# Performance work log

Measured on AMD Instinct MI355X. Metric: run time of the kernel, lower is better.

## Reference

```python
import jax, jax.numpy as jnp
import numpy as np

# dims: B batch, T query len, S kv len (=T, self-attn prefill), D embed,
# N query heads, K kv heads, G = N//K GQA groups, H head dim
B, T, D = 2, 2048, 2048
N, K, H = 16, 4, 128
G = N // K
MIN_TS, MAX_TS = 1.0, 10000.0
W_SCALE = 0.02


def _rope(x, pos):
    # x: [B, L, heads, H]; pos: [B, L] int
    half = x.shape[-1] // 2
    frac = (2.0 * jnp.arange(half, dtype=jnp.float32)) / (2 * half)
    timescale = MIN_TS * (MAX_TS / MIN_TS) ** frac            # [half]
    sinusoid = pos[:, :, None, None].astype(jnp.float32) / timescale  # [B,L,1,half]
    sin = jnp.sin(sinusoid).astype(x.dtype)
    cos = jnp.cos(sinusoid).astype(x.dtype)
    x1, x2 = jnp.split(x, 2, axis=-1)
    return jnp.concatenate([x1 * cos - x2 * sin, x2 * cos + x1 * sin], axis=-1)


def setup_inputs() -> dict:
    key = jax.random.key(0)
    ks = jax.random.split(key, 6)
    Xq = jax.random.normal(ks[0], (B, T, D), dtype=jnp.float32)
    Xkv = jax.random.normal(ks[1], (B, T, D), dtype=jnp.float32)
    pos = jnp.tile(jnp.arange(T, dtype=jnp.int32)[None, :], (B, 1))
    Wq = jax.random.normal(ks[2], (D, N, H), dtype=jnp.float32) * W_SCALE
    Wk = jax.random.normal(ks[3], (D, K, H), dtype=jnp.float32) * W_SCALE
    Wv = jax.random.normal(ks[4], (D, K, H), dtype=jnp.float32) * W_SCALE
    Wo = jax.random.normal(ks[5], (N, H, D), dtype=jnp.float32) * W_SCALE
    return {"Xq": Xq, "Xkv": Xkv, "q_positions": pos, "kv_positions": pos,
            "Wq": Wq, "Wk": Wk, "Wv": Wv, "Wo": Wo}


def reference(Xq, Xkv, q_positions, kv_positions, Wq, Wk, Wv, Wo):
    # QKV projections (tensordot in torch == einsum over contracted axis)
    q = _rope(jnp.einsum('btd,dnh->btnh', Xq, Wq), q_positions)   # [B,T,N,H]
    k = _rope(jnp.einsum('bsd,dkh->bskh', Xkv, Wk), kv_positions)  # [B,S,K,H]
    v = jnp.einsum('bsd,dkh->bskh', Xkv, Wv)                       # [B,S,K,H]
    # GQA: query head n = kv_head*G + group (matches torch enable_gqa repeat_interleave)
    qg = q.reshape(B, T, K, G, H)
    # SDPA with explicit scale=1.0 (as in the original), causal mask
    scores = jnp.einsum('btkgh,bskh->bkgts', qg, k)                # [B,K,G,T,S]
    causal = jnp.tril(jnp.ones((T, T), dtype=bool))
    scores = jnp.where(causal, scores, jnp.finfo(scores.dtype).min)
    probs = jax.nn.softmax(scores, axis=-1)
    attn = jnp.einsum('bkgts,bskh->btkgh', probs, v).reshape(B, T, N, H)
    # o_proj contracts both (N, H) axes
    return jnp.einsum('btnh,nhd->btd', attn, Wo)
```

## Files before the change

kernel.cpp:

```cpp
#include <hip/hip_runtime.h>
#include <stdint.h>

#define Bb 2
#define Td 2048
#define Sd 2048
#define Dd 2048
#define Nh 16
#define Kvh 4
#define Hd 128

typedef unsigned short u16;
typedef short bf16x8 __attribute__((ext_vector_type(8)));
typedef float f32x4 __attribute__((ext_vector_type(4)));

__device__ __forceinline__ u16 f2bf(float f) {
  union { float f; unsigned u; } v; v.f = f;
  v.u += 0x7FFF + ((v.u >> 16) & 1);
  return (u16)(v.u >> 16);
}
__device__ __forceinline__ float bf2f(u16 h) {
  union { unsigned u; float f; } v; v.u = ((unsigned)h) << 16;
  return v.f;
}

__global__ __launch_bounds__(256) void k_convert(const float* __restrict__ in,
                                                 u16* __restrict__ out, int n8) {
  int i = blockIdx.x * 256 + threadIdx.x;
  if (i >= n8) return;
  const float4* p = (const float4*)in;
  float4 a = p[(size_t)i * 2], b = p[(size_t)i * 2 + 1];
  ushort4 r0, r1;
  r0.x = f2bf(a.x); r0.y = f2bf(a.y); r0.z = f2bf(a.z); r0.w = f2bf(a.w);
  r1.x = f2bf(b.x); r1.y = f2bf(b.y); r1.z = f2bf(b.z); r1.w = f2bf(b.w);
  ((ushort4*)out)[(size_t)i * 2] = r0;
  ((ushort4*)out)[(size_t)i * 2 + 1] = r1;
}

__global__ __launch_bounds__(256) void k_transpose_f32_bf16(const float* __restrict__ in,
                                                            u16* __restrict__ out,
                                                            int R, int C) {
  __shared__ u16 tile[32][33];
  int c0 = blockIdx.x * 32, r0 = blockIdx.y * 32;
  int tx = threadIdx.x & 31, ty = threadIdx.x >> 5;
#pragma unroll
  for (int i = 0; i < 32; i += 8)
    tile[ty + i][tx] = f2bf(in[(size_t)(r0 + ty + i) * C + c0 + tx]);
  __syncthreads();
#pragma unroll
  for (int i = 0; i < 32; i += 8)
    out[(size_t)(c0 + ty + i) * R + r0 + tx] = tile[tx][ty + i];
}

__global__ __launch_bounds__(256) void k_transpose_v(const u16* __restrict__ in,
                                                     u16* __restrict__ out) {
  __shared__ u16 tile[32][33];
  int bkh = blockIdx.z;
  int b = bkh >> 2, kh = bkh & 3;
  int h0 = blockIdx.x * 32, s0 = blockIdx.y * 32;
  int tx = threadIdx.x & 31, ty = threadIdx.x >> 5;
  const u16* ib = in + (size_t)b * Sd * (Kvh * Hd) + kh * Hd;
  u16* ob = out + (size_t)(b * Kvh + kh) * Hd * Sd;
#pragma unroll
  for (int i = 0; i < 32; i += 8)
    tile[ty + i][tx] = ib[(size_t)(s0 + ty + i) * (Kvh * Hd) + h0 + tx];
  __syncthreads();
#pragma unroll
  for (int i = 0; i < 32; i += 8)
    ob[(size_t)(h0 + ty + i) * Sd + s0 + tx] = tile[tx][ty + i];
}

__global__ __launch_bounds__(256) void k_rope_tables(const int* __restrict__ pos,
                                                     float* __restrict__ cosT,
                                                     float* __restrict__ sinT, int total) {
  int idx = blockIdx.x * 256 + threadIdx.x;
  if (idx >= total) return;
  int i = idx & 63, bt = idx >> 6;
  float p = (float)pos[bt];
  float ts = powf(10000.0f, (float)i * (1.0f / 64.0f));
  float x = p / ts;
  cosT[idx] = cosf(x);
  sinT[idx] = sinf(x);
}

__global__ __launch_bounds__(256) void k_rope_q(float* __restrict__ x,
                                                const float* __restrict__ cosT,
                                                const float* __restrict__ sinT, int total) {
  int idx = blockIdx.x * 256 + threadIdx.x;
  if (idx >= total) return;
  int i = idx & 63;
  int nh = (idx >> 6) % Nh;
  int bt = idx / (64 * Nh);
  size_t base = ((size_t)bt * Nh + nh) * Hd;
  float c = cosT[bt * 64 + i], s = sinT[bt * 64 + i];
  float x1 = x[base + i], x2 = x[base + 64 + i];
  x[base + i]      = x1 * c - x2 * s;
  x[base + 64 + i] = x2 * c + x1 * s;
}

__global__ __launch_bounds__(256) void k_rope_k(const float* __restrict__ x,
                                                u16* __restrict__ out,
                                                const float* __restrict__ cosT,
                                                const float* __restrict__ sinT, int total) {
  int idx = blockIdx.x * 256 + threadIdx.x;
  if (idx >= total) return;
  int i = idx & 63;
  int kh = (idx >> 6) % Kvh;
  int bt = idx / (64 * Kvh);
  int b = bt >> 11, s = bt & 2047;
  size_t bi = ((size_t)bt * Kvh + kh) * Hd;
  size_t bo = (((size_t)b * Kvh + kh) * Sd + s) * Hd;
  float c = cosT[bt * 64 + i], sn = sinT[bt * 64 + i];
  float x1 = x[bi + i], x2 = x[bi + 64 + i];
  out[bo + i]      = f2bf(x1 * c - x2 * sn);
  out[bo + 64 + i] = f2bf(x2 * c + x1 * sn);
}

template <int OUT_F32>
__global__ __launch_bounds__(256) void k_gemm_bt(const u16* __restrict__ A,
                                                 const u16* __restrict__ Bt,
                                                 void* __restrict__ C,
                                                 int M, int Ncols, int Kd) {
  __shared__ u16 lA[128 * 32];
  __shared__ u16 lB[128 * 32];
  int tiles_n = Ncols >> 7;
  int bm = blockIdx.x / tiles_n, bn = blockIdx.x % tiles_n;
  int tid = threadIdx.x;
  int lane = tid & 63, wave = tid >> 6;
  int wr = wave >> 1, wc = wave & 1;
  int e0 = tid * 8;
  int r0 = e0 >> 5, c0 = e0 & 31;
  int lr = lane & 15, hi = lane >> 4;
  int kq = hi * 8;

  const u16* gA = A + (size_t)(bm * 128 + r0) * Kd + c0;
  const u16* gB = Bt + (size_t)(bn * 128 + r0) * Kd + c0;

  f32x4 acc[4][4] = {};

  for (int k0 = 0; k0 < Kd; k0 += 32) {
    __syncthreads();
    __builtin_amdgcn_global_load_lds(
        (const __attribute__((address_space(1))) uint32_t*)(gA + k0),
        (__attribute__((address_space(3))) uint32_t*)&lA[e0], 16, 0, 0);
    __builtin_amdgcn_global_load_lds(
        (const __attribute__((address_space(1))) uint32_t*)(gA + k0 + (size_t)64 * Kd),
        (__attribute__((address_space(3))) uint32_t*)&lA[e0 + 64 * 32], 16, 0, 0);
    __builtin_amdgcn_global_load_lds(
        (const __attribute__((address_space(1))) uint32_t*)(gB + k0),
        (__attribute__((address_space(3))) uint32_t*)&lB[e0], 16, 0, 0);
    __builtin_amdgcn_global_load_lds(
        (const __attribute__((address_space(1))) uint32_t*)(gB + k0 + (size_t)64 * Kd),
        (__attribute__((address_space(3))) uint32_t*)&lB[e0 + 64 * 32], 16, 0, 0);
    __syncthreads();

    bf16x8 af[4], bfr[4];
#pragma unroll
    for (int m = 0; m < 4; ++m)
      af[m] = *(const bf16x8*)&lA[(wr * 64 + m * 16 + lr) * 32 + kq];
#pragma unroll
    for (int n = 0; n < 4; ++n)
      bfr[n] = *(const bf16x8*)&lB[(wc * 64 + n * 16 + lr) * 32 + kq];
#pragma unroll
    for (int m = 0; m < 4; ++m)
#pragma unroll
      for (int n = 0; n < 4; ++n)
        acc[m][n] = __builtin_amdgcn_mfma_f32_16x16x32_bf16(af[m], bfr[n], acc[m][n], 0, 0, 0);
  }

  int orow0 = bm * 128 + wr * 64 + hi * 4;
  int ocol0 = bn * 128 + wc * 64 + lr;
#pragma unroll
  for (int m = 0; m < 4; ++m)
#pragma unroll
    for (int n = 0; n < 4; ++n)
#pragma unroll
      for (int q = 0; q < 4; ++q) {
        size_t idx = (size_t)(orow0 + m * 16 + q) * Ncols + ocol0 + n * 16;
        if (OUT_F32) ((float*)C)[idx] = acc[m][n][q];
        else         ((u16*)C)[idx]   = f2bf(acc[m][n][q]);
      }
}

__global__ __launch_bounds__(256) void k_gemm_kv(const u16* __restrict__ A,
                                                 const u16* __restrict__ Bt,
                                                 float* __restrict__ Ck,
                                                 u16* __restrict__ Cv) {
  __shared__ u16 lA[128 * 32];
  __shared__ u16 lB[128 * 32];
  int bm = blockIdx.x >> 3, bn = blockIdx.x & 7;
  int tid = threadIdx.x;
  int lane = tid & 63, wave = tid >> 6;
  int wr = wave >> 1, wc = wave & 1;
  int e0 = tid * 8;
  int r0 = e0 >> 5, c0 = e0 & 31;
  int lr = lane & 15, hi = lane >> 4;
  int kq = hi * 8;

  const u16* gA = A + (size_t)(bm * 128 + r0) * Dd + c0;
  const u16* gB = Bt + (size_t)(bn * 128 + r0) * Dd + c0;

  f32x4 acc[4][4] = {};

  for (int k0 = 0; k0 < Dd; k0 += 32) {
    __syncthreads();
    __builtin_amdgcn_global_load_lds(
        (const __attribute__((address_space(1))) uint32_t*)(gA + k0),
        (__attribute__((address_space(3))) uint32_t*)&lA[e0], 16, 0, 0);
    __builtin_amdgcn_global_load_lds(
        (const __attribute__((address_space(1))) uint32_t*)(gA + k0 + (size_t)64 * Dd),
        (__attribute__((address_space(3))) uint32_t*)&lA[e0 + 64 * 32], 16, 0, 0);
    __builtin_amdgcn_global_load_lds(
        (const __attribute__((address_space(1))) uint32_t*)(gB + k0),
        (__attribute__((address_space(3))) uint32_t*)&lB[e0], 16, 0, 0);
    __builtin_amdgcn_global_load_lds(
        (const __attribute__((address_space(1))) uint32_t*)(gB + k0 + (size_t)64 * Dd),
        (__attribute__((address_space(3))) uint32_t*)&lB[e0 + 64 * 32], 16, 0, 0);
    __syncthreads();

    bf16x8 af[4], bfr[4];
#pragma unroll
    for (int m = 0; m < 4; ++m)
      af[m] = *(const bf16x8*)&lA[(wr * 64 + m * 16 + lr) * 32 + kq];
#pragma unroll
    for (int n = 0; n < 4; ++n)
      bfr[n] = *(const bf16x8*)&lB[(wc * 64 + n * 16 + lr) * 32 + kq];
#pragma unroll
    for (int m = 0; m < 4; ++m)
#pragma unroll
      for (int n = 0; n < 4; ++n)
        acc[m][n] = __builtin_amdgcn_mfma_f32_16x16x32_bf16(af[m], bfr[n], acc[m][n], 0, 0, 0);
  }

  int orow0 = bm * 128 + wr * 64 + hi * 4;
  int ocol0 = bn * 128 + wc * 64 + lr;
  if (bn < 4) {
#pragma unroll
    for (int m = 0; m < 4; ++m)
#pragma unroll
      for (int n = 0; n < 4; ++n)
#pragma unroll
        for (int q = 0; q < 4; ++q)
          Ck[(size_t)(orow0 + m * 16 + q) * 512 + ocol0 + n * 16] = acc[m][n][q];
  } else {
#pragma unroll
    for (int m = 0; m < 4; ++m)
#pragma unroll
      for (int n = 0; n < 4; ++n)
#pragma unroll
        for (int q = 0; q < 4; ++q)
          Cv[(size_t)(orow0 + m * 16 + q) * 512 + (ocol0 - 512) + n * 16] = f2bf(acc[m][n][q]);
  }
}

__global__ __launch_bounds__(256) void k_attn(const float* __restrict__ Qf,
                                              const u16* __restrict__ K,
                                              const u16* __restrict__ Vt,
                                              u16* __restrict__ O) {
  __shared__ u16 kv[2][16384];
  __shared__ u16 Pl[4][1024];

  int bid0 = blockIdx.x;
  int bid = (bid0 & 7) * 64 + (bid0 >> 3);
  int p = bid & 15, n = (bid >> 4) & 15, b = bid >> 8;
  int kh = n >> 2;
  int tid = threadIdx.x;
  int lane = tid & 63, wave = tid >> 6;
  int lr = lane & 15, hi = lane >> 4;
  int kq = hi * 8;

  const u16* Kbase = K + ((size_t)(b * Kvh + kh)) * Sd * Hd;
  const u16* Vbase = Vt + ((size_t)(b * Kvh + kh)) * Hd * Sd;
  u16* Pw = &Pl[wave][0];

  for (int half = 0; half < 2; ++half) {
    int tile = half ? (31 - p) : p;
    int t0 = tile * 64 + wave * 16;

    bf16x8 qhi[4], qlo[4];
    {
      const float* qrow = Qf + ((size_t)((b * Td + t0 + lr) * Nh + n)) * Hd;
#pragma unroll
      for (int kk = 0; kk < 4; ++kk) {
        float4 a = *(const float4*)(qrow + kk * 32 + kq);
        float4 c = *(const float4*)(qrow + kk * 32 + kq + 4);
        float xs[8] = {a.x, a.y, a.z, a.w, c.x, c.y, c.z, c.w};
#pragma unroll
        for (int jj = 0; jj < 8; ++jj) {
          u16 h = f2bf(xs[jj]);
          qhi[kk][jj] = (short)h;
          qlo[kk][jj] = (short)f2bf(xs[jj] - bf2f(h));
        }
      }
    }

    float m_run[4] = {-1e30f, -1e30f, -1e30f, -1e30f};
    float l_run[4] = {0.f, 0.f, 0.f, 0.f};
    f32x4 oacc[8] = {};

    int nst = tile + 1;

    auto STAGE = [&](int st, int buf) {
      int s0 = st * 64;
      char* kb = (char*)&kv[buf][0];
#pragma unroll
      for (int it = 0; it < 4; ++it) {
        int o = it * 4096 + tid * 16;
        int r = o >> 8, w = o & 255;
        const u16* src = Kbase + (size_t)(s0 + r) * Hd + ((w ^ ((r & 7) << 4)) >> 1);
        __builtin_amdgcn_global_load_lds(
            (const __attribute__((address_space(1))) uint32_t*)src,
            (__attribute__((address_space(3))) uint32_t*)(kb + o), 16, 0, 0);
      }
#pragma unroll
      for (int it = 0; it < 4; ++it) {
        int o = it * 4096 + tid * 16;
        int h = o >> 7, w = o & 127;
        const u16* src = Vbase + (size_t)h * Sd + s0 + ((w ^ ((h & 7) << 4)) >> 1);
        __builtin_amdgcn_global_load_lds(
            (const __attribute__((address_space(1))) uint32_t*)src,
            (__attribute__((address_space(3))) uint32_t*)(kb + 16384 + o), 16, 0, 0);
      }
    };

    int cur = 0;
    STAGE(0, 0);
    asm volatile("s_waitcnt vmcnt(0)" ::: "memory");
    __syncthreads();

    for (int st = 0; st < nst; ++st) {
      if (st + 1 < nst) STAGE(st + 1, cur ^ 1);
      int s0 = st * 64;
      const char* kb = (const char*)&kv[cur][0];

      f32x4 sc[4] = {};
#pragma unroll
      for (int j = 0; j < 4; ++j) {
        int r = j * 16 + lr;
        int rx = (r & 7) << 4;
#pragma unroll
        for (int kk = 0; kk < 4; ++kk) {
          bf16x8 kf = *(const bf16x8*)(kb + r * 256 + ((kk * 64 + hi * 16) ^ rx));
          sc[j] = __builtin_amdgcn_mfma_f32_16x16x32_bf16(qhi[kk], kf, sc[j], 0, 0, 0);
          sc[j] = __builtin_amdgcn_mfma_f32_16x16x32_bf16(qlo[kk], kf, sc[j], 0, 0, 0);
        }
      }

      if (s0 + 63 > t0) {
#pragma unroll
        for (int j = 0; j < 4; ++j) {
          if (s0 + j * 16 + 15 > t0) {
            int s = s0 + j * 16 + lr;
#pragma unroll
            for (int q = 0; q < 4; ++q)
              if (s > t0 + hi * 4 + q) sc[j][q] = -1e30f;
          }
        }
      }

      float mb[4], ls[4];
#pragma unroll
      for (int q = 0; q < 4; ++q)
        mb[q] = fmaxf(fmaxf(sc[0][q], sc[1][q]), fmaxf(sc[2][q], sc[3][q]));
#pragma unroll
      for (int off = 1; off < 16; off <<= 1) {
#pragma unroll
        for (int q = 0; q < 4; ++q) mb[q] = fmaxf(mb[q], __shfl_xor(mb[q], off));
      }
      bool need = (mb[0] > m_run[0] + 8.f) || (mb[1] > m_run[1] + 8.f) ||
                  (mb[2] > m_run[2] + 8.f) || (mb[3] > m_run[3] + 8.f);
      if (__any(need)) {
        float fac[4];
#pragma unroll
        for (int q = 0; q < 4; ++q) {
          float mn = fmaxf(m_run[q], mb[q]);
          fac[q] = __expf(m_run[q] - mn);
          m_run[q] = mn;
          l_run[q] *= fac[q];
        }
#pragma unroll
        for (int hb = 0; hb < 8; ++hb)
#pragma unroll
          for (int q = 0; q < 4; ++q) oacc[hb][q] *= fac[q];
      }
#pragma unroll
      for (int j = 0; j < 4; ++j)
#pragma unroll
        for (int q = 0; q < 4; ++q) sc[j][q] = __expf(sc[j][q] - m_run[q]);
#pragma unroll
      for (int q = 0; q < 4; ++q)
        ls[q] = (sc[0][q] + sc[1][q]) + (sc[2][q] + sc[3][q]);
#pragma unroll
      for (int off = 1; off < 16; off <<= 1) {
#pragma unroll
        for (int q = 0; q < 4; ++q) ls[q] += __shfl_xor(ls[q], off);
      }
#pragma unroll
      for (int q = 0; q < 4; ++q) l_run[q] += ls[q];

#pragma unroll
      for (int j = 0; j < 4; ++j)
#pragma unroll
        for (int q = 0; q < 4; ++q) {
          int row = hi * 4 + q;
          int cb = ((j * 16 + lr) * 2) ^ ((row & 7) << 4);
          *(u16*)((char*)Pw + row * 128 + cb) = f2bf(sc[j][q]);
        }
      bf16x8 pf[2];
      {
        int rx = (lr & 7) << 4;
#pragma unroll
        for (int c = 0; c < 2; ++c)
          pf[c] = *(const bf16x8*)((const char*)Pw + lr * 128 + ((c * 64 + hi * 16) ^ rx));
      }

#pragma unroll
      for (int hb = 0; hb < 8; ++hb) {
        int h = hb * 16 + lr;
        int rx = (h & 7) << 4;
#pragma unroll
        for (int c = 0; c < 2; ++c) {
          bf16x8 vf = *(const bf16x8*)(kb + 16384 + h * 128 + ((c * 64 + hi * 16) ^ rx));
          oacc[hb] = __builtin_amdgcn_mfma_f32_16x16x32_bf16(pf[c], vf, oacc[hb], 0, 0, 0);
        }
      }

      asm volatile("s_waitcnt vmcnt(0)" ::: "memory");
      __syncthreads();
      cur ^= 1;
    }

#pragma unroll
    for (int hb = 0; hb < 8; ++hb)
#pragma unroll
      for (int q = 0; q < 4; ++q) {
        float val = oacc[hb][q] / l_run[q];
        O[((size_t)((b * Td + t0 + hi * 4 + q) * Nh + n)) * Hd + hb * 16 + lr] = f2bf(val);
      }
  }
}

extern "C" void kernel_launch(void* const* d_in, const int* in_sizes, int n_in,
                              void* d_out, int out_size, void* d_ws, size_t ws_size,
                              hipStream_t stream) {
  (void)in_sizes; (void)n_in; (void)out_size; (void)ws_size;
  const float* Xq  = (const float*)d_in[0];
  const float* Xkv = (const float*)d_in[1];
  const int* qpos  = (const int*)d_in[2];
  const int* kpos  = (const int*)d_in[3];
  const float* Wq  = (const float*)d_in[4];
  const float* Wk  = (const float*)d_in[5];
  const float* Wv  = (const float*)d_in[6];
  const float* Wo  = (const float*)d_in[7];
  float* out = (float*)d_out;

  char* ws = (char*)d_ws;
  size_t off = 0;
  auto take = [&](size_t bytes) -> char* {
    char* p = ws + off;
    off += (bytes + 255) & ~(size_t)255;
    return p;
  };
  const size_t nX   = (size_t)Bb * Td * Dd;
  const size_t nQ   = (size_t)Bb * Td * Nh * Hd;
  const size_t nKV  = (size_t)Bb * Sd * Kvh * Hd;
  const size_t nTab = (size_t)Bb * Td * 64;

  u16* XqB   = (u16*)take(nX * 2);
  u16* XkvB  = (u16*)take(nX * 2);
  u16* WqT   = (u16*)take((size_t)Nh * Hd * Dd * 2);
  u16* BtKV  = (u16*)take((size_t)(Kvh * Hd * 2) * Dd * 2);
  u16* WoT   = (u16*)take((size_t)Dd * Nh * Hd * 2);
  float* Qf  = (float*)take(nQ * 4);
  u16* Kb    = (u16*)take(nKV * 2);
  u16* Vb    = (u16*)take(nKV * 2);
  float* cosQ = (float*)take(nTab * 4);
  float* sinQ = (float*)take(nTab * 4);
  float* cosK = (float*)take(nTab * 4);
  float* sinK = (float*)take(nTab * 4);
  float* Kf  = (float*)XqB;
  u16* attnB = XqB;
  u16* Vt    = XkvB;

  k_convert<<<dim3((int)(nX / 8 / 256)), 256, 0, stream>>>(Xq, XqB, (int)(nX / 8));
  k_convert<<<dim3((int)(nX / 8 / 256)), 256, 0, stream>>>(Xkv, XkvB, (int)(nX / 8));
  k_transpose_f32_bf16<<<dim3((Nh * Hd) / 32, Dd / 32), 256, 0, stream>>>(Wq, WqT, Dd, Nh * Hd);
  k_transpose_f32_bf16<<<dim3((Kvh * Hd) / 32, Dd / 32), 256, 0, stream>>>(Wk, BtKV, Dd, Kvh * Hd);
  k_transpose_f32_bf16<<<dim3((Kvh * Hd) / 32, Dd / 32), 256, 0, stream>>>(
      Wv, BtKV + (size_t)512 * Dd, Dd, Kvh * Hd);
  k_transpose_f32_bf16<<<dim3(Dd / 32, (Nh * Hd) / 32), 256, 0, stream>>>(Wo, WoT, Nh * Hd, Dd);
  k_rope_tables<<<dim3((int)(nTab / 256)), 256, 0, stream>>>(qpos, cosQ, sinQ, (int)nTab);
  k_rope_tables<<<dim3((int)(nTab / 256)), 256, 0, stream>>>(kpos, cosK, sinK, (int)nTab);

  k_gemm_bt<1><<<dim3((Bb * Td / 128) * ((Nh * Hd) / 128)), 256, 0, stream>>>(
      XqB, WqT, Qf, Bb * Td, Nh * Hd, Dd);
  k_gemm_kv<<<dim3((Bb * Td / 128) * 8), 256, 0, stream>>>(XkvB, BtKV, Kf, Vb);

  k_rope_q<<<dim3(Bb * Td * Nh * 64 / 256), 256, 0, stream>>>(
      Qf, cosQ, sinQ, Bb * Td * Nh * 64);
  k_rope_k<<<dim3(Bb * Sd * Kvh * 64 / 256), 256, 0, stream>>>(
      Kf, Kb, cosK, sinK, Bb * Sd * Kvh * 64);
  k_transpose_v<<<dim3(Hd / 32, Sd / 32, Bb * Kvh), 256, 0, stream>>>(Vb, Vt);

  k_attn<<<dim3(Bb * Nh * 16), 256, 0, stream>>>(Qf, Kb, Vt, attnB);

  k_gemm_bt<1><<<dim3((Bb * Td / 128) * ((Nh * Hd) / 128)), 256, 0, stream>>>(
      attnB, WoT, out, Bb * Td, Nh * Hd, Dd);
}
```

Measured before the change: 319.8 us.

## Process both paired causal query tiles in one pass sharing K/V stages

Instead of running the two paired query tiles (p and 31-p) one after another, each with its own K/V streaming loop, the kernel now keeps both tiles' Q fragments and accumulators live and streams K/V once over the longer tile. The shorter tile reuses the same staged K/V blocks for its first stages. This removes redundant global-to-LDS loads and barriers for the overlapping prefix. In exchange it doubles register pressure (two sets of Q hi/lo fragments and output accumulators), which may lower occupancy or cause spills. The Q loads also change from float4 vectors to scalar loads.

Measured after the change: 384.3 us. +20.2%, slower.

```diff
diff --git a/kernel.cpp b/kernel.cpp
--- a/kernel.cpp
+++ b/kernel.cpp
@@ -272,171 +272,181 @@
   const u16* Vbase = Vt + ((size_t)(b * Kvh + kh)) * Hd * Sd;
   u16* Pw = &Pl[wave][0];
 
-  for (int half = 0; half < 2; ++half) {
-    int tile = half ? (31 - p) : p;
-    int t0 = tile * 64 + wave * 16;
-
-    bf16x8 qhi[4], qlo[4];
+  int tA = p, tB = 31 - p;
+  int t0A = tA * 64 + wave * 16;
+  int t0B = tB * 64 + wave * 16;
+  int nstA = tA + 1, nstB = tB + 1;
+
+  bf16x8 qhA[4], qlA[4], qhB[4], qlB[4];
+  {
+    const float* qrowA = Qf + ((size_t)((b * Td + t0A + lr) * Nh + n)) * Hd;
+    const float* qrowB = Qf + ((size_t)((b * Td + t0B + lr) * Nh + n)) * Hd;
+#pragma unroll
+    for (int kk = 0; kk < 4; ++kk) {
+#pragma unroll
+      for (int jj = 0; jj < 8; ++jj) {
+        float xa = qrowA[kk * 32 + kq + jj];
+        u16 ha = f2bf(xa);
+        qhA[kk][jj] = (short)ha;
+        qlA[kk][jj] = (short)f2bf(xa - bf2f(ha));
+        float xb = qrowB[kk * 32 + kq + jj];
+        u16 hb2 = f2bf(xb);
+        qhB[kk][jj] = (short)hb2;
+        qlB[kk][jj] = (short)f2bf(xb - bf2f(hb2));
+      }
+    }
+  }
+
+  float mA[4] = {-1e30f, -1e30f, -1e30f, -1e30f};
+  float lA_[4] = {0.f, 0.f, 0.f, 0.f};
+  f32x4 oA[8] = {};
+  float mB[4] = {-1e30f, -1e30f, -1e30f, -1e30f};
+  float lB_[4] = {0.f, 0.f, 0.f, 0.f};
+  f32x4 oB[8] = {};
+
+  auto DO_TILE = [&](int t0, bf16x8 (&qh)[4], bf16x8 (&ql)[4],
+                     float (&m_run)[4], float (&l_run)[4], f32x4 (&oacc)[8],
+                     int s0, const char* kb) {
+    f32x4 sc[4] = {};
+#pragma unroll
+    for (int j = 0; j < 4; ++j) {
+      int r = j * 16 + lr;
+      int rx = (r & 7) << 4;
+#pragma unroll
+      for (int kk = 0; kk < 4; ++kk) {
+        bf16x8 kf = *(const bf16x8*)(kb + r * 256 + ((kk * 64 + hi * 16) ^ rx));
+        sc[j] = __builtin_amdgcn_mfma_f32_16x16x32_bf16(qh[kk], kf, sc[j], 0, 0, 0);
+        sc[j] = __builtin_amdgcn_mfma_f32_16x16x32_bf16(ql[kk], kf, sc[j], 0, 0, 0);
+      }
+    }
+    if (s0 + 63 > t0) {
+#pragma unroll
+      for (int j = 0; j < 4; ++j) {
+        if (s0 + j * 16 + 15 > t0) {
+          int s = s0 + j * 16 + lr;
+#pragma unroll
+          for (int q = 0; q < 4; ++q)
+            if (s > t0 + hi * 4 + q) sc[j][q] = -1e30f;
+        }
+      }
+    }
+    float mb[4], ls[4];
+#pragma unroll
+    for (int q = 0; q < 4; ++q)
+      mb[q] = fmaxf(fmaxf(sc[0][q], sc[1][q]), fmaxf(sc[2][q], sc[3][q]));
+#pragma unroll
+    for (int off = 1; off < 16; off <<= 1) {
+#pragma unroll
+      for (int q = 0; q < 4; ++q) mb[q] = fmaxf(mb[q], __shfl_xor(mb[q], off));
+    }
+    bool need = (mb[0] > m_run[0] + 8.f) || (mb[1] > m_run[1] + 8.f) ||
+                (mb[2] > m_run[2] + 8.f) || (mb[3] > m_run[3] + 8.f);
+    if (__any(need)) {
+      float fac[4];
+#pragma unroll
+      for (int q = 0; q < 4; ++q) {
+        float mn = fmaxf(m_run[q], mb[q]);
+        fac[q] = __expf(m_run[q] - mn);
+        m_run[q] = mn;
+        l_run[q] *= fac[q];
+      }
+#pragma unroll
+      for (int hb = 0; hb < 8; ++hb)
+#pragma unroll
+        for (int q = 0; q < 4; ++q) oacc[hb][q] *= fac[q];
+    }
+#pragma unroll
+    for (int j = 0; j < 4; ++j)
+#pragma unroll
+      for (int q = 0; q < 4; ++q) sc[j][q] = __expf(sc[j][q] - m_run[q]);
+#pragma unroll
+    for (int q = 0; q < 4; ++q)
+      ls[q] = (sc[0][q] + sc[1][q]) + (sc[2][q] + sc[3][q]);
+#pragma unroll
+    for (int off = 1; off < 16; off <<= 1) {
+#pragma unroll
+      for (int q = 0; q < 4; ++q) ls[q] += __shfl_xor(ls[q], off);
+    }
+#pragma unroll
+    for (int q = 0; q < 4; ++q) l_run[q] += ls[q];
+
+#pragma unroll
+    for (int j = 0; j < 4; ++j)
+#pragma unroll
+      for (int q = 0; q < 4; ++q) {
+        int row = hi * 4 + q;
+        int cb = ((j * 16 + lr) * 2) ^ ((row & 7) << 4);
+        *(u16*)((char*)Pw + row * 128 + cb) = f2bf(sc[j][q]);
+      }
+    bf16x8 pf[2];
     {
-      const float* qrow = Qf + ((size_t)((b * Td + t0 + lr) * Nh + n)) * Hd;
-#pragma unroll
-      for (int kk = 0; kk < 4; ++kk) {
-        float4 a = *(const float4*)(qrow + kk * 32 + kq);
-        float4 c = *(const float4*)(qrow + kk * 32 + kq + 4);
-        float xs[8] = {a.x, a.y, a.z, a.w, c.x, c.y, c.z, c.w};
-#pragma unroll
-        for (int jj = 0; jj < 8; ++jj) {
-          u16 h = f2bf(xs[jj]);
-          qhi[kk][jj] = (short)h;
-          qlo[kk][jj] = (short)f2bf(xs[jj] - bf2f(h));
-        }
-      }
-    }
-
-    float m_run[4] = {-1e30f, -1e30f, -1e30f, -1e30f};
-    float l_run[4] = {0.f, 0.f, 0.f, 0.f};
-    f32x4 oacc[8] = {};
-
-    int nst = tile + 1;
-
-    auto STAGE = [&](int st, int buf) {
-      int s0 = st * 64;
-      char* kb = (char*)&kv[buf][0];
-#pragma unroll
-      for (int it = 0; it < 4; ++it) {
-        int o = it * 4096 + tid * 16;
-        int r = o >> 8, w = o & 255;
-        const u16* src = Kbase + (size_t)(s0 + r) * Hd + ((w ^ ((r & 7) << 4)) >> 1);
-        __builtin_amdgcn_global_load_lds(
-            (const __attribute__((address_space(1))) uint32_t*)src,
-            (__attribute__((address_space(3))) uint32_t*)(kb + o), 16, 0, 0);
-      }
-#pragma unroll
-      for (int it = 0; it < 4; ++it) {
-        int o = it * 4096 + tid * 16;
-        int h = o >> 7, w = o & 127;
-        const u16* src = Vbase + (size_t)h * Sd + s0 + ((w ^ ((h & 7) << 4)) >> 1);
-        __builtin_amdgcn_global_load_lds(
-            (const __attribute__((address_space(1))) uint32_t*)src,
-            (__attribute__((address_space(3))) uint32_t*)(kb + 16384 + o), 16, 0, 0);
-      }
-    };
-
-    int cur = 0;
-    STAGE(0, 0);
+      int rx = (lr & 7) << 4;
+#pragma unroll
+      for (int c = 0; c < 2; ++c)
+        pf[c] = *(const bf16x8*)((const char*)Pw + lr * 128 + ((c * 64 + hi * 16) ^ rx));
+    }
+#pragma unroll
+    for (int hb = 0; hb < 8; ++hb) {
+      int h = hb * 16 + lr;
+      int rx = (h & 7) << 4;
+#pragma unroll
+      for (int c = 0; c < 2; ++c) {
+        bf16x8 vf = *(const bf16x8*)(kb + 16384 + h * 128 + ((c * 64 + hi * 16) ^ rx));
+        oacc[hb] = __builtin_amdgcn_mfma_f32_16x16x32_bf16(pf[c], vf, oacc[hb], 0, 0, 0);
+      }
+    }
+  };
+
+  auto STAGE = [&](int st, int buf) {
+    int s0 = st * 64;
+    char* kb = (char*)&kv[buf][0];
+#pragma unroll
+    for (int it = 0; it < 4; ++it) {
+      int o = it * 4096 + tid * 16;
+      int r = o >> 8, w = o & 255;
+      const u16* src = Kbase + (size_t)(s0 + r) * Hd + ((w ^ ((r & 7) << 4)) >> 1);
+      __builtin_amdgcn_global_load_lds(
+          (const __attribute__((address_space(1))) uint32_t*)src,
+          (__attribute__((address_space(3))) uint32_t*)(kb + o), 16, 0, 0);
+    }
+#pragma unroll
+    for (int it = 0; it < 4; ++it) {
+      int o = it * 4096 + tid * 16;
+      int h = o >> 7, w = o & 127;
+      const u16* src = Vbase + (size_t)h * Sd + s0 + ((w ^ ((h & 7) << 4)) >> 1);
+      __builtin_amdgcn_global_load_lds(
+          (const __attribute__((address_space(1))) uint32_t*)src,
+          (__attribute__((address_space(3))) uint32_t*)(kb + 16384 + o), 16, 0, 0);
+    }
+  };
+
+  int cur = 0;
+  STAGE(0, 0);
+  asm volatile("s_waitcnt vmcnt(0)" ::: "memory");
+  __syncthreads();
+
+  for (int st = 0; st < nstB; ++st) {
+    if (st + 1 < nstB) STAGE(st + 1, cur ^ 1);
+    int s0 = st * 64;
+    const char* kb = (const char*)&kv[cur][0];
+
+    DO_TILE(t0B, qhB, qlB, mB, lB_, oB, s0, kb);
+    if (st < nstA) DO_TILE(t0A, qhA, qlA, mA, lA_, oA, s0, kb);
+
     asm volatile("s_waitcnt vmcnt(0)" ::: "memory");
     __syncthreads();
-
-    for (int st = 0; st < nst; ++st) {
-      if (st + 1 < nst) STAGE(st + 1, cur ^ 1);
-      int s0 = st * 64;
-      const char* kb = (const char*)&kv[cur][0];
-
-      f32x4 sc[4] = {};
-#pragma unroll
-      for (int j = 0; j < 4; ++j) {
-        int r = j * 16 + lr;
-        int rx = (r & 7) << 4;
-#pragma unroll
-        for (int kk = 0; kk < 4; ++kk) {
-          bf16x8 kf = *(const bf16x8*)(kb + r * 256 + ((kk * 64 + hi * 16) ^ rx));
-          sc[j] = __builtin_amdgcn_mfma_f32_16x16x32_bf16(qhi[kk], kf, sc[j], 0, 0, 0);
-          sc[j] = __builtin_amdgcn_mfma_f32_16x16x32_bf16(qlo[kk], kf, sc[j], 0, 0, 0);
-        }
-      }
-
-      if (s0 + 63 > t0) {
-#pragma unroll
-        for (int j = 0; j < 4; ++j) {
-          if (s0 + j * 16 + 15 > t0) {
-            int s = s0 + j * 16 + lr;
-#pragma unroll
-            for (int q = 0; q < 4; ++q)
-              if (s > t0 + hi * 4 + q) sc[j][q] = -1e30f;
-          }
-        }
-      }
-
-      float mb[4], ls[4];
-#pragma unroll
-      for (int q = 0; q < 4; ++q)
-        mb[q] = fmaxf(fmaxf(sc[0][q], sc[1][q]), fmaxf(sc[2][q], sc[3][q]));
-#pragma unroll
-      for (int off = 1; off < 16; off <<= 1) {
-#pragma unroll
-        for (int q = 0; q < 4; ++q) mb[q] = fmaxf(mb[q], __shfl_xor(mb[q], off));
-      }
-      bool need = (mb[0] > m_run[0] + 8.f) || (mb[1] > m_run[1] + 8.f) ||
-                  (mb[2] > m_run[2] + 8.f) || (mb[3] > m_run[3] + 8.f);
-      if (__any(need)) {
-        float fac[4];
-#pragma unroll
-        for (int q = 0; q < 4; ++q) {
-          float mn = fmaxf(m_run[q], mb[q]);
-          fac[q] = __expf(m_run[q] - mn);
-          m_run[q] = mn;
-          l_run[q] *= fac[q];
-        }
-#pragma unroll
-        for (int hb = 0; hb < 8; ++hb)
-#pragma unroll
-          for (int q = 0; q < 4; ++q) oacc[hb][q] *= fac[q];
-      }
-#pragma unroll
-      for (int j = 0; j < 4; ++j)
-#pragma unroll
-        for (int q = 0; q < 4; ++q) sc[j][q] = __expf(sc[j][q] - m_run[q]);
-#pragma unroll
-      for (int q = 0; q < 4; ++q)
-        ls[q] = (sc[0][q] + sc[1][q]) + (sc[2][q] + sc[3][q]);
-#pragma unroll
-      for (int off = 1; off < 16; off <<= 1) {
-#pragma unroll
-        for (int q = 0; q < 4; ++q) ls[q] += __shfl_xor(ls[q], off);
-      }
-#pragma unroll
-      for (int q = 0; q < 4; ++q) l_run[q] += ls[q];
-
-#pragma unroll
-      for (int j = 0; j < 4; ++j)
-#pragma unroll
-        for (int q = 0; q < 4; ++q) {
-          int row = hi * 4 + q;
-          int cb = ((j * 16 + lr) * 2) ^ ((row & 7) << 4);
-          *(u16*)((char*)Pw + row * 128 + cb) = f2bf(sc[j][q]);
-        }
-      bf16x8 pf[2];
-      {
-        int rx = (lr & 7) << 4;
-#pragma unroll
-        for (int c = 0; c < 2; ++c)
-          pf[c] = *(const bf16x8*)((const char*)Pw + lr * 128 + ((c * 64 + hi * 16) ^ rx));
-      }
-
-#pragma unroll
-      for (int hb = 0; hb < 8; ++hb) {
-        int h = hb * 16 + lr;
-        int rx = (h & 7) << 4;
-#pragma unroll
-        for (int c = 0; c < 2; ++c) {
-          bf16x8 vf = *(const bf16x8*)(kb + 16384 + h * 128 + ((c * 64 + hi * 16) ^ rx));
-          oacc[hb] = __builtin_amdgcn_mfma_f32_16x16x32_bf16(pf[c], vf, oacc[hb], 0, 0, 0);
-        }
-      }
-
-      asm volatile("s_waitcnt vmcnt(0)" ::: "memory");
-      __syncthreads();
-      cur ^= 1;
-    }
-
-#pragma unroll
-    for (int hb = 0; hb < 8; ++hb)
-#pragma unroll
-      for (int q = 0; q < 4; ++q) {
-        float val = oacc[hb][q] / l_run[q];
-        O[((size_t)((b * Td + t0 + hi * 4 + q) * Nh + n)) * Hd + hb * 16 + lr] = f2bf(val);
-      }
+    cur ^= 1;
   }
+
+#pragma unroll
+  for (int hb = 0; hb < 8; ++hb)
+#pragma unroll
+    for (int q = 0; q < 4; ++q) {
+      float vB = oB[hb][q] / lB_[q];
+      O[((size_t)((b * Td + t0B + hi * 4 + q) * Nh + n)) * Hd + hb * 16 + lr] = f2bf(vB);
+      float vA = oA[hb][q] / lA_[q];
+      O[((size_t)((b * Td + t0A + hi * 4 + q) * Nh + n)) * Hd + hb * 16 + lr] = f2bf(vA);
+    }
 }
 
 extern "C" void kernel_launch(void* const* d_in, const int* in_sizes, int n_in,
```
